# Kernel tuning notes

Hardware: AMD Instinct MI355X
Metric: run time of the kernel (lower is better)

Reference implementation:

```python
import jax, jax.numpy as jnp
import numpy as np

DIM = 768
NUM_HEADS = 12
HEAD_DIM = DIM // NUM_HEADS
SCALE = HEAD_DIM ** -0.5


def setup_inputs() -> dict:
    key = jax.random.key(0)
    ks = jax.random.split(key, 12)
    B, N, C, H = 8, 1024, DIM, NUM_HEADS
    s = 0.02
    return {
        'q_in': jax.random.normal(ks[0], (B, N, C), jnp.float32),
        'kv_in': jax.random.normal(ks[1], (B, N, C), jnp.float32),
        'Wq': jax.random.normal(ks[2], (C, C), jnp.float32) * s,
        'Wk': jax.random.normal(ks[3], (C, C), jnp.float32) * s,
        'Wv': jax.random.normal(ks[4], (C, C), jnp.float32) * s,
        'Wp': jax.random.normal(ks[5], (C, C), jnp.float32) * s,
        'bp': jnp.zeros((C,), jnp.float32),
        'W_dy2': jax.random.normal(ks[6], (H, C), jnp.float32) * s,  # lf gate linear (out=H)
        'b_dy2': jnp.zeros((H,), jnp.float32),
        'W_dy': jax.random.normal(ks[7], (H, C), jnp.float32) * s,   # hf gate linear
        'b_dy': jnp.zeros((H,), jnp.float32),
        'lf_gamma': jnp.full((C,), 1e-5, jnp.float32),
        'hf_gamma': jnp.full((C,), 1e-5, jnp.float32),
        'star_scale': jnp.ones((1,), jnp.float32),
        'star_bias': jnp.zeros((1,), jnp.float32),
    }


def reference(q_in, kv_in, Wq, Wk, Wv, Wp, bp, W_dy2, b_dy2, W_dy, b_dy,
              lf_gamma, hf_gamma, star_scale, star_bias):
    B, Nq, C = q_in.shape
    Nk = kv_in.shape[1]
    H, D = NUM_HEADS, HEAD_DIM

    # StarReLU on query tokens (ignore_cls_token = 0)
    dy_feat = star_scale * jnp.square(jax.nn.relu(q_in)) + star_bias  # (B,Nq,C)

    # low-freq dynamic gate: tanh(linear) per head, repeated over head_dim
    dy_lf = jnp.tanh(jnp.einsum('bnc,hc->bnh', dy_feat, W_dy2) + b_dy2)  # (B,Nq,H)
    dy_lf = jnp.repeat(dy_lf, D, axis=-1)  # (B,Nq,C)

    # high-freq dynamic gate: rational-of-softplus^2
    dy = jax.nn.softplus(jnp.einsum('bnc,hc->bnh', dy_feat, W_dy) + b_dy)
    dy2 = jnp.square(dy)
    dy_hf = 2.0 * dy2 / (dy2 + 0.3678)
    dy_hf = jnp.repeat(dy_hf, D, axis=-1)  # (B,Nq,C)

    # projections (torch Linear: y = x @ W.T), split heads
    q = jnp.einsum('bnc,dc->bnd', q_in, Wq).reshape(B, Nq, H, D).transpose(0, 2, 1, 3)
    k = jnp.einsum('bnc,dc->bnd', kv_in, Wk).reshape(B, Nk, H, D).transpose(0, 2, 1, 3)
    v = jnp.einsum('bnc,dc->bnd', kv_in, Wv).reshape(B, Nk, H, D).transpose(0, 2, 1, 3)

    attn = jnp.einsum('bhqd,bhkd->bhqk', q * SCALE, k)
    attn = jax.nn.softmax(attn, axis=-1)
    x_attn = jnp.einsum('bhqk,bhkd->bhqd', attn, v)
    x_attn = x_attn.transpose(0, 2, 1, 3).reshape(B, Nq, C)

    # Nk == Nq branch: per-token residual high-frequency component
    v_reshape = v.transpose(0, 2, 1, 3).reshape(B, Nk, C)
    v_hf = v_reshape - x_attn

    x_attn = x_attn + x_attn * dy_lf * lf_gamma
    x_attn = x_attn + dy_hf * v_hf * hf_gamma

    out = jnp.einsum('bnc,dc->bnd', x_attn, Wp) + bp
    return out
```

## Files before the change

kernel.cpp:

```cpp
#include <hip/hip_runtime.h>
#include <hip/hip_bf16.h>
#include <stdint.h>

typedef unsigned short u16;
typedef unsigned int u32;
typedef unsigned long long u64;
typedef __attribute__((ext_vector_type(8))) short short8;
typedef __attribute__((ext_vector_type(4))) float f32x4;

#define LOG2E 1.44269504f

static __device__ __forceinline__ u16 f2bf(float f) {
    u32 x = __float_as_uint(f);
    u32 r = (x + 0x7FFFu + ((x >> 16) & 1u)) >> 16;
    return (u16)r;
}
static __device__ __forceinline__ float bf2f(u16 u) {
    return __uint_as_float(((u32)u) << 16);
}
static __device__ __forceinline__ u32 pk2(float lo, float hi) {
    __hip_bfloat162 t = __float22bfloat162_rn(float2{lo, hi});
    union { __hip_bfloat162 b; u32 u; } cv;
    cv.b = t;
    return cv.u;
}
static __device__ __forceinline__ float fexp2(float x) {
#if __has_builtin(__builtin_amdgcn_exp2f)
    return __builtin_amdgcn_exp2f(x);
#else
    return exp2f(x);
#endif
}

static __device__ __forceinline__ void g2l16(const void* g, void* l) {
    __builtin_amdgcn_global_load_lds((const __attribute__((address_space(1))) void*)g,
                                     (__attribute__((address_space(3))) void*)l, 16, 0, 0);
}

__global__ __launch_bounds__(256) void k_cvt_all(
    const float* __restrict__ q_in, const float* __restrict__ kv_in,
    const float* __restrict__ Wq, const float* __restrict__ Wk,
    const float* __restrict__ Wv, const float* __restrict__ Wp,
    const float* __restrict__ Wdy2, const float* __restrict__ Wdy,
    u16* __restrict__ qbf, u16* __restrict__ kvbf, u16* __restrict__ Wqb,
    u16* __restrict__ Wkb, u16* __restrict__ Wvb, u16* __restrict__ Wpb,
    u16* __restrict__ wgb) {
    int i = blockIdx.x * 256 + threadIdx.x;
    const float* src;
    u16* dst;
    int so, dofs;
    if (i < 786432) { src = q_in; dst = qbf; so = i; dofs = i; }
    else if (i < 1572864) { src = kv_in; dst = kvbf; so = i - 786432; dofs = so; }
    else if (i < 1646592) { src = Wq; dst = Wqb; so = i - 1572864; dofs = so; }
    else if (i < 1720320) { src = Wk; dst = Wkb; so = i - 1646592; dofs = so; }
    else if (i < 1794048) { src = Wv; dst = Wvb; so = i - 1720320; dofs = so; }
    else if (i < 1867776) { src = Wp; dst = Wpb; so = i - 1794048; dofs = so; }
    else if (i < 1870080) {
        int e = i - 1867776;
        dst = wgb; dofs = e;
        if (e < 1152) { src = Wdy2; so = e; }
        else { src = Wdy; so = e - 1152; }
    } else return;
    const float4* p = (const float4*)src + (size_t)so * 2;
    float4 a = p[0], b = p[1];
    short8 o;
    o[0] = f2bf(a.x); o[1] = f2bf(a.y); o[2] = f2bf(a.z); o[3] = f2bf(a.w);
    o[4] = f2bf(b.x); o[5] = f2bf(b.y); o[6] = f2bf(b.z); o[7] = f2bf(b.w);
    *((short8*)dst + dofs) = o;
}

__global__ __launch_bounds__(64) void k_gates(
    const u16* __restrict__ qbf, const u16* __restrict__ wgb,
    const float* __restrict__ bdy2, const float* __restrict__ bdy,
    const float* __restrict__ star_s, const float* __restrict__ star_b,
    float* __restrict__ glf, float* __restrict__ ghf) {
    int lane = threadIdx.x;
    int g = lane >> 4, c = lane & 15;
    int row0 = blockIdx.x * 16;
    float ss = star_s[0], sb = star_b[0];
    f32x4 acc[2];
    acc[0] = (f32x4){0.f, 0.f, 0.f, 0.f};
    acc[1] = (f32x4){0.f, 0.f, 0.f, 0.f};
    for (int t = 0; t < 24; ++t) {
        int k0 = t * 32;
        short8 x8 = *(const short8*)(qbf + (size_t)(row0 + c) * 768 + k0 + g * 8);
        float f[8];
#pragma unroll
        for (int j = 0; j < 8; ++j) {
            float x = fmaxf(bf2f((u16)x8[j]), 0.f);
            f[j] = ss * x * x + sb;
        }
        union { u32 u[4]; short8 s8; } au;
#pragma unroll
        for (int j = 0; j < 4; ++j) au.u[j] = pk2(f[2 * j], f[2 * j + 1]);
        short8 b0 = *(const short8*)(wgb + (size_t)c * 768 + k0 + g * 8);
        short8 b1 = (short8){0, 0, 0, 0, 0, 0, 0, 0};
        if (c < 8)
            b1 = *(const short8*)(wgb + (size_t)(16 + c) * 768 + k0 + g * 8);
        acc[0] = __builtin_amdgcn_mfma_f32_16x16x32_bf16(au.s8, b0, acc[0], 0, 0, 0);
        acc[1] = __builtin_amdgcn_mfma_f32_16x16x32_bf16(au.s8, b1, acc[1], 0, 0, 0);
    }
#pragma unroll
    for (int n = 0; n < 2; ++n)
#pragma unroll
        for (int r = 0; r < 4; ++r) {
            int token = row0 + g * 4 + r;
            int o = n * 16 + c;
            float v = acc[n][r];
            if (o < 12) {
                glf[(size_t)token * 12 + o] = tanhf(v + bdy2[o]);
            } else if (o < 24) {
                float x = v + bdy[o - 12];
                float sp = (x > 15.f) ? x : log1pf(expf(x));
                float d2 = sp * sp;
                ghf[(size_t)token * 12 + (o - 12)] = 2.f * d2 / (d2 + 0.3678f);
            }
        }
}

__device__ __forceinline__ void gemm_core(const u16* __restrict__ A,
                                          const u16* __restrict__ W, u16* As,
                                          u16* Bs, int rowA0, int rowB0,
                                          int lane, int w, int wm, int wn,
                                          f32x4 acc[4][4]) {
    int g = lane >> 4, c = lane & 15;
#pragma unroll
    for (int m = 0; m < 4; ++m)
#pragma unroll
        for (int n = 0; n < 4; ++n) acc[m][n] = (f32x4){0.f, 0.f, 0.f, 0.f};

    auto stage = [&](int buf, int k0) {
#pragma unroll
        for (int j = 0; j < 2; ++j) {
            int L = w * 128 + j * 64 + lane;
            int p = L >> 3, s8 = L & 7;
            int t2 = s8 ^ (p & 7);
            int row = 2 * p + (t2 >> 2);
            int chunk = t2 & 3;
            size_t go = (size_t)row * 768 + k0 + chunk * 8;
            g2l16(A + (size_t)rowA0 * 768 + go, As + buf * 4096 + L * 8);
            g2l16(W + (size_t)rowB0 * 768 + go, Bs + buf * 4096 + L * 8);
        }
    };

    stage(0, 0);
    __syncthreads();
    int buf = 0;
    for (int t = 0; t < 24; ++t) {
        if (t < 23) stage(buf ^ 1, (t + 1) * 32);
        short8 a[4], b[4];
#pragma unroll
        for (int m = 0; m < 4; ++m) {
            int row = wm * 64 + m * 16 + c;
            int off = (row >> 1) * 64 +
                      ((((row & 1) << 2) | g) ^ ((row >> 1) & 7)) * 8;
            a[m] = *(const short8*)(As + buf * 4096 + off);
        }
#pragma unroll
        for (int n = 0; n < 4; ++n) {
            int row = wn * 64 + n * 16 + c;
            int off = (row >> 1) * 64 +
                      ((((row & 1) << 2) | g) ^ ((row >> 1) & 7)) * 8;
            b[n] = *(const short8*)(Bs + buf * 4096 + off);
        }
#pragma unroll
        for (int m = 0; m < 4; ++m)
#pragma unroll
            for (int n = 0; n < 4; ++n)
                acc[m][n] = __builtin_amdgcn_mfma_f32_16x16x32_bf16(
                    a[m], b[n], acc[m][n], 0, 0, 0);
        __syncthreads();
        buf ^= 1;
    }
}

__global__ __launch_bounds__(256, 2) void k_gemm_qkv(
    const u16* __restrict__ qbf, const u16* __restrict__ kvbf,
    const u16* __restrict__ Wqb, const u16* __restrict__ Wkb,
    const u16* __restrict__ Wvb, u16* __restrict__ Qb, u16* __restrict__ Kb,
    u16* __restrict__ VTg, u16* __restrict__ vlin) {
    __shared__ __align__(16) u16 smem[16384];
    u16* As = smem;
    u16* Bs = smem + 8192;
    int bid = blockIdx.x;
    int logical = (bid & 7) * 144 + (bid >> 3);
    int panel = logical / 18, sub = logical % 18;
    int type = sub / 6, tn = sub % 6;
    int tid = threadIdx.x, lane = tid & 63, w = tid >> 6;
    int g = lane >> 4, c = lane & 15;
    int wm = w >> 1, wn = w & 1;
    int rowA0 = panel * 128, rowB0 = tn * 128;
    const u16* A = (type == 0) ? qbf : kvbf;
    const u16* W = (type == 0) ? Wqb : (type == 1) ? Wkb : Wvb;

    f32x4 acc[4][4];
    gemm_core(A, W, As, Bs, rowA0, rowB0, lane, w, wm, wn, acc);

    if (type == 0) {
        const float scl = 0.125f * LOG2E;
#pragma unroll
        for (int m = 0; m < 4; ++m)
#pragma unroll
            for (int n = 0; n < 4; ++n)
#pragma unroll
                for (int r = 0; r < 4; ++r) {
                    int row = rowA0 + wm * 64 + m * 16 + g * 4 + r;
                    int col = rowB0 + wn * 64 + n * 16 + c;
                    int bb = row >> 10, nn = row & 1023, hh = col >> 6,
                        dd = col & 63;
                    Qb[((size_t)(bb * 12 + hh) << 16) + (nn << 6) + dd] =
                        f2bf(acc[m][n][r] * scl);
                }
    } else if (type == 1) {
#pragma unroll
        for (int m = 0; m < 4; ++m)
#pragma unroll
            for (int n = 0; n < 4; ++n)
#pragma unroll
                for (int r = 0; r < 4; ++r) {
                    int row = rowA0 + wm * 64 + m * 16 + g * 4 + r;
                    int col = rowB0 + wn * 64 + n * 16 + c;
                    int bb = row >> 10, nn = row & 1023, hh = col >> 6,
                        dd = col & 63;
                    Kb[((size_t)(bb * 12 + hh) << 16) + (nn << 6) + dd] =
                        f2bf(acc[m][n][r]);
                }
    } else {
#pragma unroll
        for (int m = 0; m < 4; ++m)
#pragma unroll
            for (int n = 0; n < 4; ++n)
#pragma unroll
                for (int r = 0; r < 4; ++r) {
                    int row = rowA0 + wm * 64 + m * 16 + g * 4 + r;
                    int col = rowB0 + wn * 64 + n * 16 + c;
                    vlin[(size_t)row * 768 + col] = f2bf(acc[m][n][r]);
                }
        __syncthreads();
#pragma unroll
        for (int m = 0; m < 4; ++m)
#pragma unroll
            for (int n = 0; n < 4; ++n)
#pragma unroll
                for (int r = 0; r < 4; ++r) {
                    int rl = wm * 64 + m * 16 + g * 4 + r;
                    int cl = wn * 64 + n * 16 + c;
                    smem[cl * 128 + rl] = f2bf(acc[m][n][r]);
                }
        __syncthreads();
        int bb = rowA0 >> 10, nn0 = rowA0 & 1023;
#pragma unroll
        for (int j = 0; j < 8; ++j) {
            int idx = j * 256 + tid;
            int rT = idx >> 4, cc = idx & 15;
            int dout = rowB0 + rT, hh = dout >> 6, dd = dout & 63;
            const u16* srow = smem + rT * 128 + cc * 8;
            size_t robase = ((size_t)(bb * 12 + hh) * 64 + dd) * 1024;
#pragma unroll
            for (int e2 = 0; e2 < 4; ++e2) {
                int n0 = nn0 + cc * 8 + 2 * e2;
                int t6 = n0 & 63;
                int pos = (((t6 >> 1) & 1) << 5) | (((t6 >> 2) & 3) << 3) |
                          (((t6 >> 4) & 3) << 1) | (t6 & 1);
                u32 val = (u32)srow[2 * e2] | ((u32)srow[2 * e2 + 1] << 16);
                *(u32*)(VTg + robase + (n0 & ~63) + pos) = val;
            }
        }
    }
}

__global__ __launch_bounds__(256, 2) void k_gemm_out(
    const u16* __restrict__ xf, const u16* __restrict__ Wpb,
    const float* __restrict__ bp, float* __restrict__ out) {
    __shared__ __align__(16) u16 smem[16384];
    u16* As = smem;
    u16* Bs = smem + 8192;
    int bid = blockIdx.x;
    int logical = (bid & 7) * 48 + (bid >> 3);
    int c48 = logical % 48;
    int tm = (logical / 48) * 8 + c48 / 6, tn = c48 % 6;
    int tid = threadIdx.x, lane = tid & 63, w = tid >> 6;
    int wm = w >> 1, wn = w & 1;
    int rowA0 = tm * 128, rowB0 = tn * 128;

    f32x4 acc[4][4];
    gemm_core(xf, Wpb, As, Bs, rowA0, rowB0, lane, w, wm, wn, acc);

#pragma unroll
    for (int m = 0; m < 4; ++m)
#pragma unroll
        for (int n = 0; n < 4; ++n)
#pragma unroll
            for (int r = 0; r < 4; ++r) {
                int row = rowA0 + wm * 64 + m * 16 + (lane >> 4) * 4 + r;
                int col = rowB0 + wn * 64 + n * 16 + (lane & 15);
                out[(size_t)row * 768 + col] = acc[m][n][r] + bp[col];
            }
}

__global__ __launch_bounds__(256, 2) void k_attn(
    const u16* __restrict__ Qb, const u16* __restrict__ Kb,
    const u16* __restrict__ VTg, const u16* __restrict__ vlin,
    const float* __restrict__ glf, const float* __restrict__ ghf,
    const float* __restrict__ lfg, const float* __restrict__ hfg,
    u16* __restrict__ xfinal) {
    __shared__ __align__(16) u16 Ks[2][4096];
    __shared__ __align__(16) u16 Vs[2][4096];
    int b8 = blockIdx.x;
    int sw = (b8 & 7) * 96 + (b8 >> 3);
    int bh = sw >> 3, qblk = sw & 7;
    int bb = bh / 12, hh = bh % 12;
    int tid = threadIdx.x, lane = tid & 63, w = tid >> 6;
    int g = lane >> 4, c = lane & 15;
    const char* Kp = (const char*)(Kb + ((size_t)bh << 16));
    const char* Vp = (const char*)(VTg + ((size_t)bh << 16));
    const u16* Qp = Qb + ((size_t)bh << 16);
    int q0 = qblk * 128 + w * 32;

    short8 qf[2][2];
#pragma unroll
    for (int qb = 0; qb < 2; ++qb)
#pragma unroll
        for (int ks = 0; ks < 2; ++ks)
            qf[qb][ks] = *(const short8*)(Qp + (size_t)(q0 + qb * 16 + c) * 64 +
                                          ks * 32 + g * 8);

    f32x4 o[2][4];
#pragma unroll
    for (int qb = 0; qb < 2; ++qb)
#pragma unroll
        for (int n = 0; n < 4; ++n) o[qb][n] = (f32x4){0.f, 0.f, 0.f, 0.f};
    f32x4 o5[2];
    o5[0] = (f32x4){0.f, 0.f, 0.f, 0.f};
    o5[1] = (f32x4){0.f, 0.f, 0.f, 0.f};
    const short8 vones = (short8){(short)0x3F80, (short)0x3F80, (short)0x3F80,
                                  (short)0x3F80, (short)0x3F80, (short)0x3F80,
                                  (short)0x3F80, (short)0x3F80};

    int kgo[2], vgo[2], ldo[2];
#pragma unroll
    for (int h = 0; h < 2; ++h) {
        int idx = w * 64 + lane + h * 256;
        int row = idx >> 3;
        int colb = ((idx & 7) * 16) ^ ((row & 7) << 4);
        kgo[h] = row * 128 + colb;
        vgo[h] = row * 2048 + colb;
        ldo[h] = (w * 64 + h * 256) * 16;
    }

    auto stage = [&](int bi, int t) {
#pragma unroll
        for (int h = 0; h < 2; ++h) {
            g2l16(Kp + (size_t)t * 8192 + kgo[h], (char*)&Ks[bi][0] + ldo[h]);
            g2l16(Vp + (size_t)t * 128 + vgo[h], (char*)&Vs[bi][0] + ldo[h]);
        }
    };

    stage(0, 0);
    __syncthreads();
    int buf = 0;
    int cs = (c & 7) << 4;
    for (int t = 0; t < 16; ++t) {
        if (t < 15) stage(buf ^ 1, t + 1);
        const char* Kbase = (const char*)&Ks[buf][0];
        const char* Vbase = (const char*)&Vs[buf][0];
        short8 kf[4][2], vf[4][2];
#pragma unroll
        for (int m = 0; m < 4; ++m) {
            int rowb = (m * 16 + c) * 128;
#pragma unroll
            for (int ks = 0; ks < 2; ++ks)
                kf[m][ks] = *(const short8*)(Kbase + rowb +
                                             ((g * 16 + ks * 64) ^ cs));
        }
#pragma unroll
        for (int n = 0; n < 4; ++n) {
            int rowb = (n * 16 + c) * 128;
#pragma unroll
            for (int a = 0; a < 2; ++a)
                vf[n][a] = *(const short8*)(Vbase + rowb +
                                            ((a * 64 + g * 16) ^ cs));
        }
#pragma unroll
        for (int qb = 0; qb < 2; ++qb) {
            f32x4 s[4];
            __builtin_amdgcn_s_setprio(1);
#pragma unroll
            for (int m = 0; m < 4; ++m) {
                s[m] = __builtin_amdgcn_mfma_f32_16x16x32_bf16(
                    kf[m][0], qf[qb][0], (f32x4){0.f, 0.f, 0.f, 0.f}, 0, 0, 0);
                s[m] = __builtin_amdgcn_mfma_f32_16x16x32_bf16(
                    kf[m][1], qf[qb][1], s[m], 0, 0, 0);
            }
            __builtin_amdgcn_s_setprio(0);
            u32 P2[4][2];
#pragma unroll
            for (int m = 0; m < 4; ++m) {
#pragma unroll
                for (int r = 0; r < 4; ++r) s[m][r] = fexp2(s[m][r]);
                P2[m][0] = pk2(s[m][0], s[m][1]);
                P2[m][1] = pk2(s[m][2], s[m][3]);
            }
#pragma unroll
            for (int a = 0; a < 2; ++a) {
                union { u32 u[4]; short8 s8; } pu;
                pu.u[0] = P2[0][a]; pu.u[1] = P2[1][a];
                pu.u[2] = P2[2][a]; pu.u[3] = P2[3][a];
                __builtin_amdgcn_s_setprio(1);
#pragma unroll
                for (int n = 0; n < 4; ++n)
                    o[qb][n] = __builtin_amdgcn_mfma_f32_16x16x32_bf16(
                        pu.s8, vf[n][a], o[qb][n], 0, 0, 0);
                o5[qb] = __builtin_amdgcn_mfma_f32_16x16x32_bf16(
                    pu.s8, vones, o5[qb], 0, 0, 0);
                __builtin_amdgcn_s_setprio(0);
            }
        }
        __syncthreads();
        buf ^= 1;
    }

    u16* X = &Ks[0][0];
#pragma unroll
    for (int qb = 0; qb < 2; ++qb) {
        float rl[4];
#pragma unroll
        for (int r = 0; r < 4; ++r) rl[r] = 1.0f / o5[qb][r];
#pragma unroll
        for (int n = 0; n < 4; ++n)
#pragma unroll
            for (int r = 0; r < 4; ++r) {
                int row = w * 32 + qb * 16 + 4 * g + r;
                int col = n * 16 + c;
                int byte = row * 128 + ((col * 2) ^ ((row & 3) << 4));
                *(u16*)((char*)X + byte) = f2bf(o[qb][n][r] * rl[r]);
            }
    }
    __syncthreads();
    {
        int row = tid >> 1, half = tid & 1;
        size_t token = (size_t)bb * 1024 + qblk * 128 + row;
        float alf = glf[token * 12 + hh];
        float ahf = ghf[token * 12 + hh];
        int dbase = hh * 64 + half * 32;
        const u16* vbase = vlin + token * 768 + dbase;
        u16* obase = xfinal + token * 768 + dbase;
#pragma unroll
        for (int j = 0; j < 4; ++j) {
            int phys = ((half * 4 + j) ^ (row & 3)) * 16;
            short8 xa8 = *(const short8*)((char*)X + row * 128 + phys);
            short8 vl8 = *(const short8*)(vbase + j * 8);
            float4 lg0 = *(const float4*)(lfg + dbase + j * 8);
            float4 lg1 = *(const float4*)(lfg + dbase + j * 8 + 4);
            float4 hg0 = *(const float4*)(hfg + dbase + j * 8);
            float4 hg1 = *(const float4*)(hfg + dbase + j * 8 + 4);
            float lg[8] = {lg0.x, lg0.y, lg0.z, lg0.w, lg1.x, lg1.y, lg1.z, lg1.w};
            float hg[8] = {hg0.x, hg0.y, hg0.z, hg0.w, hg1.x, hg1.y, hg1.z, hg1.w};
            short8 oo;
#pragma unroll
            for (int e = 0; e < 8; ++e) {
                float xa = bf2f((u16)xa8[e]);
                float v = bf2f((u16)vl8[e]);
                float val = xa + xa * alf * lg[e] + ahf * (v - xa) * hg[e];
                oo[e] = f2bf(val);
            }
            *(short8*)(obase + j * 8) = oo;
        }
    }
}

extern "C" void kernel_launch(void* const* d_in, const int* in_sizes, int n_in,
                              void* d_out, int out_size, void* d_ws,
                              size_t ws_size, hipStream_t stream) {
    const float* q_in = (const float*)d_in[0];
    const float* kv_in = (const float*)d_in[1];
    const float* Wq = (const float*)d_in[2];
    const float* Wk = (const float*)d_in[3];
    const float* Wv = (const float*)d_in[4];
    const float* Wp = (const float*)d_in[5];
    const float* bp = (const float*)d_in[6];
    const float* Wdy2 = (const float*)d_in[7];
    const float* bdy2 = (const float*)d_in[8];
    const float* Wdy = (const float*)d_in[9];
    const float* bdy = (const float*)d_in[10];
    const float* lfg = (const float*)d_in[11];
    const float* hfg = (const float*)d_in[12];
    const float* st_s = (const float*)d_in[13];
    const float* st_b = (const float*)d_in[14];
    float* out = (float*)d_out;

    char* ws = (char*)d_ws;
    const size_t MC2 = (size_t)8192 * 768 * 2;
    const size_t WB = (size_t)768 * 768 * 2;
    u16* qbf = (u16*)(ws);
    u16* kvbf = (u16*)(ws + MC2);
    u16* Wqb = (u16*)(ws + 2 * MC2);
    u16* Wkb = (u16*)(ws + 2 * MC2 + WB);
    u16* Wvb = (u16*)(ws + 2 * MC2 + 2 * WB);
    u16* Wpb = (u16*)(ws + 2 * MC2 + 3 * WB);
    u16* Qb = (u16*)(ws + 2 * MC2 + 4 * WB);
    u16* Kb = (u16*)(ws + 3 * MC2 + 4 * WB);
    u16* VTg = (u16*)(ws + 4 * MC2 + 4 * WB);
    u16* vlin = (u16*)(ws + 5 * MC2 + 4 * WB);
    float* glf = (float*)(ws + 6 * MC2 + 4 * WB);
    float* ghf = (float*)(ws + 6 * MC2 + 4 * WB + (size_t)8192 * 12 * 4);
    u16* wgb = (u16*)(ws + 6 * MC2 + 4 * WB + (size_t)8192 * 12 * 8);
    u16* xfinal = qbf;

    k_cvt_all<<<7305, 256, 0, stream>>>(q_in, kv_in, Wq, Wk, Wv, Wp, Wdy2,
                                        Wdy, qbf, kvbf, Wqb, Wkb, Wvb, Wpb,
                                        wgb);
    k_gates<<<512, 64, 0, stream>>>(qbf, wgb, bdy2, bdy, st_s, st_b, glf, ghf);
    k_gemm_qkv<<<1152, 256, 0, stream>>>(qbf, kvbf, Wqb, Wkb, Wvb, Qb, Kb,
                                         VTg, vlin);
    k_attn<<<768, 256, 0, stream>>>(Qb, Kb, VTg, vlin, glf, ghf, lfg, hfg,
                                    xfinal);
    k_gemm_out<<<384, 256, 0, stream>>>(xfinal, Wpb, bp, out);
}
```

Baseline: 138.6 us.

## Triple-buffer LDS staging with vmcnt waits and one barrier per step

```diff
diff --git a/kernel.cpp b/kernel.cpp
--- a/kernel.cpp
+++ b/kernel.cpp
@@ -144,44 +144,49 @@
     };
 
     stage(0, 0);
-    __syncthreads();
-    int buf = 0;
+    stage(1, 32);
+    int cur = 0, nxt = 2;
     for (int t = 0; t < 24; ++t) {
-        if (t < 23) stage(buf ^ 1, (t + 1) * 32);
+        if (t < 23) asm volatile("s_waitcnt vmcnt(4)" ::: "memory");
+        else        asm volatile("s_waitcnt vmcnt(0)" ::: "memory");
+        __builtin_amdgcn_s_barrier();
+        if (t < 22) stage(nxt, (t + 2) * 32);
         short8 a[4], b[4];
 #pragma unroll
         for (int m = 0; m < 4; ++m) {
             int row = wm * 64 + m * 16 + c;
             int off = (row >> 1) * 64 +
                       ((((row & 1) << 2) | g) ^ ((row >> 1) & 7)) * 8;
-            a[m] = *(const short8*)(As + buf * 4096 + off);
+            a[m] = *(const short8*)(As + cur * 4096 + off);
         }
 #pragma unroll
         for (int n = 0; n < 4; ++n) {
             int row = wn * 64 + n * 16 + c;
             int off = (row >> 1) * 64 +
                       ((((row & 1) << 2) | g) ^ ((row >> 1) & 7)) * 8;
-            b[n] = *(const short8*)(Bs + buf * 4096 + off);
-        }
+            b[n] = *(const short8*)(Bs + cur * 4096 + off);
+        }
+        __builtin_amdgcn_s_setprio(1);
 #pragma unroll
         for (int m = 0; m < 4; ++m)
 #pragma unroll
             for (int n = 0; n < 4; ++n)
                 acc[m][n] = __builtin_amdgcn_mfma_f32_16x16x32_bf16(
                     a[m], b[n], acc[m][n], 0, 0, 0);
-        __syncthreads();
-        buf ^= 1;
-    }
-}
-
-__global__ __launch_bounds__(256, 2) void k_gemm_qkv(
+        __builtin_amdgcn_s_setprio(0);
+        cur = (cur == 2) ? 0 : cur + 1;
+        nxt = (nxt == 2) ? 0 : nxt + 1;
+    }
+}
+
+__global__ __launch_bounds__(256, 3) void k_gemm_qkv(
     const u16* __restrict__ qbf, const u16* __restrict__ kvbf,
     const u16* __restrict__ Wqb, const u16* __restrict__ Wkb,
     const u16* __restrict__ Wvb, u16* __restrict__ Qb, u16* __restrict__ Kb,
     u16* __restrict__ VTg, u16* __restrict__ vlin) {
-    __shared__ __align__(16) u16 smem[16384];
+    __shared__ __align__(16) u16 smem[24576];
     u16* As = smem;
-    u16* Bs = smem + 8192;
+    u16* Bs = smem + 12288;
     int bid = blockIdx.x;
     int logical = (bid & 7) * 144 + (bid >> 3);
     int panel = logical / 18, sub = logical % 18;
@@ -269,12 +274,12 @@
     }
 }
 
-__global__ __launch_bounds__(256, 2) void k_gemm_out(
+__global__ __launch_bounds__(256, 3) void k_gemm_out(
     const u16* __restrict__ xf, const u16* __restrict__ Wpb,
     const float* __restrict__ bp, float* __restrict__ out) {
-    __shared__ __align__(16) u16 smem[16384];
+    __shared__ __align__(16) u16 smem[24576];
     u16* As = smem;
-    u16* Bs = smem + 8192;
+    u16* Bs = smem + 12288;
     int bid = blockIdx.x;
     int logical = (bid & 7) * 48 + (bid >> 3);
     int c48 = logical % 48;
@@ -298,14 +303,14 @@
             }
 }
 
-__global__ __launch_bounds__(256, 2) void k_attn(
+__global__ __launch_bounds__(256, 3) void k_attn(
     const u16* __restrict__ Qb, const u16* __restrict__ Kb,
     const u16* __restrict__ VTg, const u16* __restrict__ vlin,
     const float* __restrict__ glf, const float* __restrict__ ghf,
     const float* __restrict__ lfg, const float* __restrict__ hfg,
     u16* __restrict__ xfinal) {
-    __shared__ __align__(16) u16 Ks[2][4096];
-    __shared__ __align__(16) u16 Vs[2][4096];
+    __shared__ __align__(16) u16 Ks[12288];
+    __shared__ __align__(16) u16 Vs[12288];
     int b8 = blockIdx.x;
     int sw = (b8 & 7) * 96 + (b8 >> 3);
     int bh = sw >> 3, qblk = sw & 7;
@@ -351,19 +356,22 @@
     auto stage = [&](int bi, int t) {
 #pragma unroll
         for (int h = 0; h < 2; ++h) {
-            g2l16(Kp + (size_t)t * 8192 + kgo[h], (char*)&Ks[bi][0] + ldo[h]);
-            g2l16(Vp + (size_t)t * 128 + vgo[h], (char*)&Vs[bi][0] + ldo[h]);
+            g2l16(Kp + (size_t)t * 8192 + kgo[h], (char*)Ks + bi * 8192 + ldo[h]);
+            g2l16(Vp + (size_t)t * 128 + vgo[h], (char*)Vs + bi * 8192 + ldo[h]);
         }
     };
 
     stage(0, 0);
-    __syncthreads();
-    int buf = 0;
+    stage(1, 1);
+    int cur = 0, nxt = 2;
     int cs = (c & 7) << 4;
     for (int t = 0; t < 16; ++t) {
-        if (t < 15) stage(buf ^ 1, t + 1);
-        const char* Kbase = (const char*)&Ks[buf][0];
-        const char* Vbase = (const char*)&Vs[buf][0];
+        if (t < 15) asm volatile("s_waitcnt vmcnt(4)" ::: "memory");
+        else        asm volatile("s_waitcnt vmcnt(0)" ::: "memory");
+        __builtin_amdgcn_s_barrier();
+        if (t < 14) stage(nxt, t + 2);
+        const char* Kbase = (const char*)Ks + cur * 8192;
+        const char* Vbase = (const char*)Vs + cur * 8192;
         short8 kf[4][2], vf[4][2];
 #pragma unroll
         for (int m = 0; m < 4; ++m) {
@@ -416,11 +424,12 @@
                 __builtin_amdgcn_s_setprio(0);
             }
         }
-        __syncthreads();
-        buf ^= 1;
-    }
-
-    u16* X = &Ks[0][0];
+        cur = (cur == 2) ? 0 : cur + 1;
+        nxt = (nxt == 2) ? 0 : nxt + 1;
+    }
+    __syncthreads();
+
+    u16* X = &Ks[0];
 #pragma unroll
     for (int qb = 0; qb < 2; ++qb) {
         float rl[4];
```

Result: faster. 134.2 us (-3.1%).
